# Optimization experiments

Hardware: AMD Instinct MI355X
Metric: run time of the kernel (lower is better)

The kernel has to match this reference:

```python
import jax, jax.numpy as jnp
import numpy as np

N, E, B, IN, H = 50000, 800000, 256, 1024, 256


def setup_inputs() -> dict:
    key = jax.random.key(0)
    ks = iter(jax.random.split(key, 40))
    w = lambda *s: jax.random.normal(next(ks), s, jnp.float32) * 0.05
    z = lambda *s: jnp.zeros(s, jnp.float32)
    inp = {
        "x": jax.random.normal(next(ks), (N, IN), jnp.float32),
        "edge_index": jax.random.randint(next(ks), (2, E), 0, N),
        "batch": jnp.sort(jax.random.randint(next(ks), (N,), 0, B)),
        "y": jax.random.randint(next(ks), (B,), 0, 2),
        "perm": jax.random.permutation(next(ks), B),
        # masker params
        "m_fc_w": w(IN, H), "m_fc_b": z(H),
        "m_c1_w": w(H, H), "m_c1_b": z(H),
        "m_c2_w": w(H, H), "m_c2_b": z(H),
        "m_node_w": w(H, 1), "m_node_b": z(1),
        "m_edge_w": w(2 * H, 1), "m_edge_b": z(1),
        # gnn_c params
        "c_fc_w": w(IN, H), "c_fc_b": z(H),
        "c_c1_w": w(H, H), "c_c1_b": z(H),
        "c_c2_w": w(H, H), "c_c2_b": z(H),
        # gnn_b params
        "b_fc_w": w(IN, H), "b_fc_b": z(H),
        "b_c1_w": w(H, H), "b_c1_b": z(H),
        "b_c2_w": w(H, H), "b_c2_b": z(H),
        # classifier heads
        "mlp_c_w": w(2 * H, 2), "mlp_c_b": z(2),
        "mlp_b_w": w(2 * H, 2), "mlp_b_b": z(2),
    }
    return inp


def _gcn_conv(x, w, b, row, col, ew):
    """PyG GCNConv: linear -> add self-loops -> sym-norm -> scatter-add -> bias."""
    n = x.shape[0]
    xw = x @ w
    loop = jnp.arange(n)
    r = jnp.concatenate([row, loop])
    c = jnp.concatenate([col, loop])
    if ew is None:
        ewf = jnp.ones(r.shape[0], xw.dtype)
    else:
        ewf = jnp.concatenate([ew, jnp.ones(n, xw.dtype)])
    deg = jax.ops.segment_sum(ewf, c, num_segments=n)
    dis = jnp.where(deg > 0, jax.lax.rsqrt(jnp.maximum(deg, 1e-12)), 0.0)
    norm = dis[r] * ewf * dis[c]
    out = jax.ops.segment_sum(xw[r] * norm[:, None], c, num_segments=n)
    return out + b


def _gnn_net(x, row, col, batch, node_mask, edge_mask, fc_w, fc_b, c1w, c1b, c2w, c2b):
    h = x * node_mask
    h = h @ fc_w + fc_b
    h = jax.nn.relu(_gcn_conv(h, c1w, c1b, row, col, edge_mask))
    h = jax.nn.relu(_gcn_conv(h, c2w, c2b, row, col, edge_mask))
    s = jax.ops.segment_sum(h, batch, num_segments=B)
    cnt = jax.ops.segment_sum(jnp.ones(h.shape[0], h.dtype), batch, num_segments=B)
    return s / jnp.maximum(cnt, 1.0)[:, None]


def _ce(logits, y):
    return -jnp.take_along_axis(jax.nn.log_softmax(logits, -1), y[:, None], 1)[:, 0]


def _gce(logits, y, q=0.7):
    p = jax.nn.softmax(logits, -1)
    yg = jnp.take_along_axis(p, y[:, None], 1)[:, 0]
    return _ce(logits, y) * (jax.lax.stop_gradient(yg) ** q) * q


def reference(x, edge_index, batch, y, perm,
              m_fc_w, m_fc_b, m_c1_w, m_c1_b, m_c2_w, m_c2_b,
              m_node_w, m_node_b, m_edge_w, m_edge_b,
              c_fc_w, c_fc_b, c_c1_w, c_c1_b, c_c2_w, c_c2_b,
              b_fc_w, b_fc_b, b_c1_w, b_c1_b, b_c2_w, b_c2_b,
              mlp_c_w, mlp_c_b, mlp_b_w, mlp_b_b):
    sg = jax.lax.stop_gradient
    row, col = edge_index[0], edge_index[1]

    # ---- GCNMasker (dropout = eval identity) ----
    h = x @ m_fc_w + m_fc_b
    h = jax.nn.relu(_gcn_conv(h, m_c1_w, m_c1_b, row, col, None))
    h = jax.nn.relu(_gcn_conv(h, m_c2_w, m_c2_b, row, col, None))
    node_score_c = jax.nn.sigmoid(h @ m_node_w + m_node_b)          # [N,1]
    # cat([x[row],x[col]]) @ W == (x @ W_top)[row] + (x @ W_bot)[col]
    es = (h @ m_edge_w[:H])[row] + (h @ m_edge_w[H:])[col] + m_edge_b
    edge_score_c = jax.nn.sigmoid(es)                               # [E,1]
    edge_score_b = 1.0 - edge_score_c
    node_score_b = 1.0 - node_score_c

    score_c = _gnn_net(x, row, col, batch, node_score_c, edge_score_c[:, 0],
                       c_fc_w, c_fc_b, c_c1_w, c_c1_b, c_c2_w, c_c2_b)  # [B,H]
    score_b = _gnn_net(x, row, col, batch, node_score_b, edge_score_b[:, 0],
                       b_fc_w, b_fc_b, b_c1_w, b_c1_b, b_c2_w, b_c2_b)  # [B,H]

    z_c = jnp.concatenate([score_c, sg(score_b)], axis=1)
    z_b = jnp.concatenate([sg(score_c), score_b], axis=1)
    pred_c = z_c @ mlp_c_w + mlp_c_b
    pred_b = z_b @ mlp_b_w + mlp_b_b

    loss_dis = _ce(pred_c, y).mean() + _gce(pred_b, y).mean()

    z_b_swap = score_b[perm]
    label_swap = y[perm]
    z_mix_conflict = jnp.concatenate([score_c, sg(z_b_swap)], axis=1)
    z_mix_align = jnp.concatenate([sg(score_c), z_b_swap], axis=1)
    pred_mix_conflict = z_mix_conflict @ mlp_c_w + mlp_c_b
    pred_mix_align = z_mix_align @ mlp_b_w + mlp_b_b
    loss_swap = _ce(pred_mix_conflict, y).mean() + _gce(pred_mix_align, label_swap).mean()

    lambda_swap = 15.0
    loss = loss_dis + lambda_swap * loss_swap
    return pred_c, loss
```

## Files before the change

kernel.cpp:

```cpp
#include <hip/hip_runtime.h>
#include <cstdint>
#include <cstddef>

#define N_NODES 50000
#define N_EDGES 800000
#define NB      256
#define IN_DIM  1024
#define HDIM    256

typedef __attribute__((ext_vector_type(8))) short bf16x8;
typedef __attribute__((ext_vector_type(4))) short s4v;
typedef __attribute__((ext_vector_type(4))) float f32x4;

__device__ __forceinline__ float sigmoidf_(float v) { return 1.0f / (1.0f + expf(-v)); }

__device__ __forceinline__ short f2bf(float f) {
    unsigned u = __float_as_uint(f);
    unsigned r = (u + 0x7FFFu + ((u >> 16) & 1u)) >> 16;
    return (short)r;
}
__device__ __forceinline__ float bf2f(short s) {
    return __uint_as_float(((unsigned)(unsigned short)s) << 16);
}

__global__ void k_hist(const int* __restrict__ col, int* __restrict__ cnt, int n) {
    int e = blockIdx.x * 256 + threadIdx.x;
    if (e < n) atomicAdd(&cnt[col[e]], 1);
}

__global__ void k_scan1(const int* __restrict__ cnt, int* __restrict__ ptr,
                        int* __restrict__ bsums, int n) {
    __shared__ int sh[256];
    int t = threadIdx.x;
    int base = blockIdx.x * 2048 + t * 8;
    int v[8]; int s = 0;
#pragma unroll
    for (int i = 0; i < 8; ++i) { int idx = base + i; v[i] = (idx < n) ? cnt[idx] : 0; s += v[i]; }
    sh[t] = s;
    __syncthreads();
    for (int off = 1; off < 256; off <<= 1) {
        int x = (t >= off) ? sh[t - off] : 0;
        __syncthreads();
        sh[t] += x;
        __syncthreads();
    }
    int excl = sh[t] - s;
    if (t == 255) bsums[blockIdx.x] = sh[255];
    int run = excl;
#pragma unroll
    for (int i = 0; i < 8; ++i) { int idx = base + i; if (idx < n) ptr[idx] = run; run += v[i]; }
}

__global__ void k_scan2(int* __restrict__ bsums, int nb, int* __restrict__ ptr_n) {
    if (threadIdx.x == 0 && blockIdx.x == 0) {
        int run = 0;
        for (int i = 0; i < nb; ++i) { int v = bsums[i]; bsums[i] = run; run += v; }
        ptr_n[0] = run;
    }
}

__global__ void k_scan3(int* __restrict__ ptr, const int* __restrict__ bsums, int n) {
    int base = blockIdx.x * 2048 + threadIdx.x * 8;
    int add = bsums[blockIdx.x];
#pragma unroll
    for (int i = 0; i < 8; ++i) { int idx = base + i; if (idx < n) ptr[idx] += add; }
}

__global__ void k_copy_int(const int* __restrict__ a, int* __restrict__ b, int n) {
    int i = blockIdx.x * 256 + threadIdx.x;
    if (i < n) b[i] = a[i];
}

__global__ void k_scatter(const int* __restrict__ row, const int* __restrict__ col,
                          int* __restrict__ fill, int* __restrict__ src,
                          int* __restrict__ eid, int n) {
    int e = blockIdx.x * 256 + threadIdx.x;
    if (e < n) {
        int c = col[e];
        int p = atomicAdd(&fill[c], 1);
        src[p] = row[e];
        eid[p] = e;
    }
}

__global__ void k_dis1(const int* __restrict__ ptr, float* __restrict__ dis, int n) {
    int i = blockIdx.x * 256 + threadIdx.x;
    if (i < n) {
        float deg = 1.0f + (float)(ptr[i + 1] - ptr[i]);
        dis[i] = 1.0f / sqrtf(deg);
    }
}

__global__ void k_splitB(const float* __restrict__ W, short* __restrict__ bt_hi,
                         short* __restrict__ bt_lo, int K, int nOff) {
    int idx = blockIdx.x * 256 + threadIdx.x;
    if (idx >= 256 * (K >> 2)) return;
    int n = idx & 255, kq = (idx >> 8) << 2;
    s4v h, l;
#pragma unroll
    for (int j = 0; j < 4; ++j) {
        float v = W[(size_t)(kq + j) * 256 + n];
        short hh = f2bf(v);
        h[j] = hh;
        l[j] = f2bf(v - bf2f(hh));
    }
    *reinterpret_cast<s4v*>(&bt_hi[(size_t)(nOff + n) * K + kq]) = h;
    *reinterpret_cast<s4v*>(&bt_lo[(size_t)(nOff + n) * K + kq]) = l;
}

template <int AMODE, int SCALE, int OUTK>
__global__ __launch_bounds__(256, 2) void k_gemm(const float* __restrict__ A32,
                                                 const short* __restrict__ AHg,
                                                 const short* __restrict__ ALg,
                                                 const short* __restrict__ BtHi,
                                                 const short* __restrict__ BtLo,
                                                 const float* __restrict__ nsv,
                                                 const float* __restrict__ kbias,
                                                 const float* __restrict__ cbias,
                                                 float* __restrict__ C32,
                                                 short* __restrict__ CHg,
                                                 short* __restrict__ CLg,
                                                 float* __restrict__ Cf1,
                                                 float* __restrict__ Cf2,
                                                 int M, int K) {
    __shared__ short Ah[128 * 32];
    __shared__ short Al[128 * 32];
    __shared__ short Bh[128 * 32];
    __shared__ short Bl[128 * 32];

    const int tid = threadIdx.x;
    const int lane = tid & 63;
    const int wave = tid >> 6;
    const int wr = wave >> 1, wc = wave & 1;
    const int lr = lane & 15, kg = lane >> 4;
    const int m0 = blockIdx.y * 128, n0 = blockIdx.x * 128;
    const int sw = (lr >> 1) & 3;

    f32x4 acc[4][4] = {};

    float4 pa[4]; float ps[4]; float4 pkb[4];
    int4 pah[2], pal[2];
    int4 pbh[2], pbl[2];

    const int NT = K >> 5;

    auto LOAD = [&](int t) {
        const int k0 = t << 5;
        if constexpr (AMODE == 0) {
#pragma unroll
            for (int i = 0; i < 4; ++i) {
                int u = tid + i * 256;
                int rowi = u >> 3, kq = (u & 7) << 2;
                int gr = m0 + rowi;
                float4 av = make_float4(0.f, 0.f, 0.f, 0.f);
                float s = 1.f;
                float4 kb = make_float4(0.f, 0.f, 0.f, 0.f);
                if (gr < M) {
                    av = *reinterpret_cast<const float4*>(A32 + (size_t)gr * K + k0 + kq);
                    if constexpr (SCALE == 1) s = nsv[gr];
                    if constexpr (SCALE == 2) s = 1.f - nsv[gr];
                    if constexpr (SCALE != 0)
                        kb = *reinterpret_cast<const float4*>(kbias + k0 + kq);
                }
                pa[i] = av; ps[i] = s; pkb[i] = kb;
            }
        } else {
#pragma unroll
            for (int i = 0; i < 2; ++i) {
                int u = tid + i * 256;
                int rowi = u >> 2, ch = u & 3;
                int gr = m0 + rowi;
                int4 h = make_int4(0, 0, 0, 0), l = make_int4(0, 0, 0, 0);
                if (gr < M) {
                    size_t g = (size_t)gr * K + k0 + (ch << 3);
                    h = *reinterpret_cast<const int4*>(AHg + g);
                    l = *reinterpret_cast<const int4*>(ALg + g);
                }
                pah[i] = h; pal[i] = l;
            }
        }
#pragma unroll
        for (int i = 0; i < 2; ++i) {
            int u = tid + i * 256;
            int rowi = u >> 2, ch = u & 3;
            size_t g = (size_t)(n0 + rowi) * K + k0 + (ch << 3);
            pbh[i] = *reinterpret_cast<const int4*>(BtHi + g);
            pbl[i] = *reinterpret_cast<const int4*>(BtLo + g);
        }
    };

    auto STORE = [&]() {
        if constexpr (AMODE == 0) {
#pragma unroll
            for (int i = 0; i < 4; ++i) {
                int u = tid + i * 256;
                int rowi = u >> 3, kq = (u & 7) << 2;
                float4 av = pa[i];
                if constexpr (SCALE != 0) {
                    float s = ps[i]; float4 kb = pkb[i];
                    av.x = fmaf(s, av.x, kb.x);
                    av.y = fmaf(s, av.y, kb.y);
                    av.z = fmaf(s, av.z, kb.z);
                    av.w = fmaf(s, av.w, kb.w);
                }
                short hx = f2bf(av.x), hy = f2bf(av.y), hz = f2bf(av.z), hw = f2bf(av.w);
                s4v h = {hx, hy, hz, hw};
                s4v l = {f2bf(av.x - bf2f(hx)), f2bf(av.y - bf2f(hy)),
                         f2bf(av.z - bf2f(hz)), f2bf(av.w - bf2f(hw))};
                int g = kq >> 3, hf = kq & 7;
                int base = rowi * 32 + ((g ^ ((rowi >> 1) & 3)) << 3) + hf;
                *reinterpret_cast<s4v*>(&Ah[base]) = h;
                *reinterpret_cast<s4v*>(&Al[base]) = l;
            }
        } else {
#pragma unroll
            for (int i = 0; i < 2; ++i) {
                int u = tid + i * 256;
                int rowi = u >> 2, ch = u & 3;
                int base = rowi * 32 + ((ch ^ ((rowi >> 1) & 3)) << 3);
                *reinterpret_cast<int4*>(&Ah[base]) = pah[i];
                *reinterpret_cast<int4*>(&Al[base]) = pal[i];
            }
        }
#pragma unroll
        for (int i = 0; i < 2; ++i) {
            int u = tid + i * 256;
            int rowi = u >> 2, ch = u & 3;
            int base = rowi * 32 + ((ch ^ ((rowi >> 1) & 3)) << 3);
            *reinterpret_cast<int4*>(&Bh[base]) = pbh[i];
            *reinterpret_cast<int4*>(&Bl[base]) = pbl[i];
        }
    };

    LOAD(0);
    STORE();
    __syncthreads();

    for (int t = 0; t < NT; ++t) {
        if (t + 1 < NT) LOAD(t + 1);

        bf16x8 a_h[4], a_l[4], b_h[4], b_l[4];
#pragma unroll
        for (int i = 0; i < 4; ++i) {
            int ar = wr * 64 + i * 16 + lr;
            int aoff = ar * 32 + ((kg ^ sw) << 3);
            a_h[i] = *reinterpret_cast<const bf16x8*>(&Ah[aoff]);
            a_l[i] = *reinterpret_cast<const bf16x8*>(&Al[aoff]);
            int br = wc * 64 + i * 16 + lr;
            int boff = br * 32 + ((kg ^ sw) << 3);
            b_h[i] = *reinterpret_cast<const bf16x8*>(&Bh[boff]);
            b_l[i] = *reinterpret_cast<const bf16x8*>(&Bl[boff]);
        }
#pragma unroll
        for (int i = 0; i < 4; ++i)
#pragma unroll
            for (int j = 0; j < 4; ++j) {
                acc[i][j] = __builtin_amdgcn_mfma_f32_16x16x32_bf16(a_h[i], b_h[j], acc[i][j], 0, 0, 0);
                acc[i][j] = __builtin_amdgcn_mfma_f32_16x16x32_bf16(a_h[i], b_l[j], acc[i][j], 0, 0, 0);
                acc[i][j] = __builtin_amdgcn_mfma_f32_16x16x32_bf16(a_l[i], b_h[j], acc[i][j], 0, 0, 0);
            }
        __syncthreads();
        if (t + 1 < NT) STORE();
        __syncthreads();
    }

#pragma unroll
    for (int i = 0; i < 4; ++i) {
#pragma unroll
        for (int j = 0; j < 4; ++j) {
#pragma unroll
            for (int r = 0; r < 4; ++r) {
                int gr = m0 + wr * 64 + i * 16 + kg * 4 + r;
                if (gr >= M) continue;
                int gc = n0 + wc * 64 + j * 16 + lr;
                float v = acc[i][j][r];
                if constexpr (OUTK == 0) {
                    C32[(size_t)gr * 256 + gc] = v;
                } else {
                    int seg = gc >> 8, c = gc & 255;
                    if (seg == 0) {
                        v += cbias[c];
                        short h = f2bf(v);
                        CHg[(size_t)gr * 256 + c] = h;
                        CLg[(size_t)gr * 256 + c] = f2bf(v - bf2f(h));
                    } else if (seg == 1) {
                        Cf1[(size_t)gr * 256 + c] = v;
                    } else {
                        Cf2[(size_t)gr * 256 + c] = v;
                    }
                }
            }
        }
    }
}

template <int MODE, int OUT>
__global__ __launch_bounds__(256) void k_conv(const float* __restrict__ xw,
                                              const float* __restrict__ dis,
                                              const float* __restrict__ ew,
                                              const int* __restrict__ ptr,
                                              const int* __restrict__ srcA,
                                              const int* __restrict__ eidA,
                                              const float* __restrict__ bias,
                                              float* __restrict__ out32,
                                              short* __restrict__ outH,
                                              short* __restrict__ outL) {
    int node = blockIdx.x * 4 + (threadIdx.x >> 6);
    if (node >= N_NODES) return;
    int lane = threadIdx.x & 63;
    const float4* xw4 = reinterpret_cast<const float4*>(xw);
    int s = ptr[node], e = ptr[node + 1];
    float4 acc = make_float4(0.f, 0.f, 0.f, 0.f);
    int k = s;
    for (; k + 2 <= e; k += 2) {
        int sr0 = srcA[k], sr1 = srcA[k + 1];
        float w0 = dis[sr0], w1 = dis[sr1];
        if (MODE == 1) { w0 *= ew[eidA[k]]; w1 *= ew[eidA[k + 1]]; }
        else if (MODE == 2) { w0 *= (1.0f - ew[eidA[k]]); w1 *= (1.0f - ew[eidA[k + 1]]); }
        float4 v0 = xw4[(size_t)sr0 * 64 + lane];
        float4 v1 = xw4[(size_t)sr1 * 64 + lane];
        acc.x = fmaf(w1, v1.x, fmaf(w0, v0.x, acc.x));
        acc.y = fmaf(w1, v1.y, fmaf(w0, v0.y, acc.y));
        acc.z = fmaf(w1, v1.z, fmaf(w0, v0.z, acc.z));
        acc.w = fmaf(w1, v1.w, fmaf(w0, v0.w, acc.w));
    }
    if (k < e) {
        int sr = srcA[k];
        float w = dis[sr];
        if (MODE == 1) w *= ew[eidA[k]];
        else if (MODE == 2) w *= (1.0f - ew[eidA[k]]);
        float4 v = xw4[(size_t)sr * 64 + lane];
        acc.x = fmaf(w, v.x, acc.x);
        acc.y = fmaf(w, v.y, acc.y);
        acc.z = fmaf(w, v.z, acc.z);
        acc.w = fmaf(w, v.w, acc.w);
    }
    float di = dis[node];
    float4 xv = xw4[(size_t)node * 64 + lane];
    float4 bv = reinterpret_cast<const float4*>(bias)[lane];
    float ox = fmaxf(fmaf(di, acc.x + di * xv.x, bv.x), 0.0f);
    float oy = fmaxf(fmaf(di, acc.y + di * xv.y, bv.y), 0.0f);
    float oz = fmaxf(fmaf(di, acc.z + di * xv.z, bv.z), 0.0f);
    float ow = fmaxf(fmaf(di, acc.w + di * xv.w, bv.w), 0.0f);
    size_t o4 = (size_t)node * 64 + lane;
    if constexpr (OUT == 0) {
        reinterpret_cast<float4*>(out32)[o4] = make_float4(ox, oy, oz, ow);
    } else {
        short hx = f2bf(ox), hy = f2bf(oy), hz = f2bf(oz), hw = f2bf(ow);
        s4v h = {hx, hy, hz, hw};
        s4v l = {f2bf(ox - bf2f(hx)), f2bf(oy - bf2f(hy)),
                 f2bf(oz - bf2f(hz)), f2bf(ow - bf2f(hw))};
        reinterpret_cast<s4v*>(outH)[o4] = h;
        reinterpret_cast<s4v*>(outL)[o4] = l;
    }
}

__global__ __launch_bounds__(256) void k_nodescore(const short* __restrict__ Sh,
                                                   const short* __restrict__ Sl,
                                                   const float* __restrict__ node_w,
                                                   const float* __restrict__ node_b,
                                                   const float* __restrict__ edge_w,
                                                   float* __restrict__ ns,
                                                   float* __restrict__ en1,
                                                   float* __restrict__ en2) {
    int node = blockIdx.x * 4 + (threadIdx.x >> 6);
    if (node >= N_NODES) return;
    int lane = threadIdx.x & 63;
    size_t o4 = (size_t)node * 64 + lane;
    s4v hh = reinterpret_cast<const s4v*>(Sh)[o4];
    s4v hl = reinterpret_cast<const s4v*>(Sl)[o4];
    float4 hv = make_float4(bf2f(hh[0]) + bf2f(hl[0]), bf2f(hh[1]) + bf2f(hl[1]),
                            bf2f(hh[2]) + bf2f(hl[2]), bf2f(hh[3]) + bf2f(hl[3]));
    float4 w1 = reinterpret_cast<const float4*>(node_w)[lane];
    float4 w2 = reinterpret_cast<const float4*>(edge_w)[lane];
    float4 w3 = reinterpret_cast<const float4*>(edge_w)[64 + lane];
    float d1 = hv.x * w1.x + hv.y * w1.y + hv.z * w1.z + hv.w * w1.w;
    float d2 = hv.x * w2.x + hv.y * w2.y + hv.z * w2.z + hv.w * w2.w;
    float d3 = hv.x * w3.x + hv.y * w3.y + hv.z * w3.z + hv.w * w3.w;
#pragma unroll
    for (int off = 32; off > 0; off >>= 1) {
        d1 += __shfl_xor(d1, off);
        d2 += __shfl_xor(d2, off);
        d3 += __shfl_xor(d3, off);
    }
    if (lane == 0) {
        ns[node] = sigmoidf_(d1 + node_b[0]);
        en1[node] = d2;
        en2[node] = d3;
    }
}

__global__ void k_edgescore(const int* __restrict__ row, const int* __restrict__ col,
                            const float* __restrict__ en1, const float* __restrict__ en2,
                            const float* __restrict__ eb, float* __restrict__ esc, int n) {
    int e = blockIdx.x * 256 + threadIdx.x;
    if (e < n) esc[e] = sigmoidf_(en1[row[e]] + en2[col[e]] + eb[0]);
}

__global__ void k_degcb(const int* __restrict__ ptr, const int* __restrict__ eidA,
                        const float* __restrict__ esc, float* __restrict__ dis_c,
                        float* __restrict__ dis_b, int n) {
    int i = blockIdx.x * 256 + threadIdx.x;
    if (i >= n) return;
    int s = ptr[i], e = ptr[i + 1];
    float t = 0.f;
    for (int k = s; k < e; ++k) t += esc[eidA[k]];
    float indeg = (float)(e - s);
    dis_c[i] = 1.0f / sqrtf(1.0f + t);
    dis_b[i] = 1.0f / sqrtf(1.0f + (indeg - t));
}

__global__ void k_starts(const int* __restrict__ batch, int* __restrict__ starts) {
    int b = threadIdx.x;
    if (b > NB) return;
    int lo = 0, hi = N_NODES;
    while (lo < hi) { int mid = (lo + hi) >> 1; if (batch[mid] < b) lo = mid + 1; else hi = mid; }
    starts[b] = lo;
}

__global__ __launch_bounds__(256) void k_pool(const float* __restrict__ h,
                                              const int* __restrict__ starts,
                                              float* __restrict__ out) {
    int b = blockIdx.x, ch = threadIdx.x;
    int s = starts[b], e = starts[b + 1];
    float acc = 0.f;
    for (int i = s; i < e; ++i) acc += h[(size_t)i * HDIM + ch];
    out[b * HDIM + ch] = acc / fmaxf((float)(e - s), 1.0f);
}

__global__ __launch_bounds__(64) void k_head(const float* __restrict__ score_c,
                                             const float* __restrict__ score_b,
                                             const int* __restrict__ y,
                                             const int* __restrict__ perm,
                                             const float* __restrict__ wc,
                                             const float* __restrict__ bc,
                                             const float* __restrict__ wb,
                                             const float* __restrict__ bb,
                                             float* __restrict__ pred_out,
                                             float* __restrict__ loss_part) {
    int b = blockIdx.x, lane = threadIdx.x;
    int pidx = perm[b];
    float4 vc = reinterpret_cast<const float4*>(score_c)[b * 64 + lane];
    float4 vb = reinterpret_cast<const float4*>(score_b)[b * 64 + lane];
    float4 vp = reinterpret_cast<const float4*>(score_b)[pidx * 64 + lane];
    const float4* wc4 = reinterpret_cast<const float4*>(wc);
    const float4* wb4 = reinterpret_cast<const float4*>(wb);
    float4 cA0 = wc4[lane * 2], cA1 = wc4[lane * 2 + 1];
    float4 cB0 = wc4[128 + lane * 2], cB1 = wc4[128 + lane * 2 + 1];
    float4 bA0 = wb4[lane * 2], bA1 = wb4[lane * 2 + 1];
    float4 bB0 = wb4[128 + lane * 2], bB1 = wb4[128 + lane * 2 + 1];

    float c1_0 = vc.x * cA0.x + vc.y * cA0.z + vc.z * cA1.x + vc.w * cA1.z;
    float c1_1 = vc.x * cA0.y + vc.y * cA0.w + vc.z * cA1.y + vc.w * cA1.w;
    float c2_0 = vb.x * cB0.x + vb.y * cB0.z + vb.z * cB1.x + vb.w * cB1.z;
    float c2_1 = vb.x * cB0.y + vb.y * cB0.w + vb.z * cB1.y + vb.w * cB1.w;
    float cp_0 = vp.x * cB0.x + vp.y * cB0.z + vp.z * cB1.x + vp.w * cB1.z;
    float cp_1 = vp.x * cB0.y + vp.y * cB0.w + vp.z * cB1.y + vp.w * cB1.w;
    float b1_0 = vc.x * bA0.x + vc.y * bA0.z + vc.z * bA1.x + vc.w * bA1.z;
    float b1_1 = vc.x * bA0.y + vc.y * bA0.w + vc.z * bA1.y + vc.w * bA1.w;
    float b2_0 = vb.x * bB0.x + vb.y * bB0.z + vb.z * bB1.x + vb.w * bB1.z;
    float b2_1 = vb.x * bB0.y + vb.y * bB0.w + vb.z * bB1.y + vb.w * bB1.w;
    float bp_0 = vp.x * bB0.x + vp.y * bB0.z + vp.z * bB1.x + vp.w * bB1.z;
    float bp_1 = vp.x * bB0.y + vp.y * bB0.w + vp.z * bB1.y + vp.w * bB1.w;

#pragma unroll
    for (int off = 32; off > 0; off >>= 1) {
        c1_0 += __shfl_xor(c1_0, off); c1_1 += __shfl_xor(c1_1, off);
        c2_0 += __shfl_xor(c2_0, off); c2_1 += __shfl_xor(c2_1, off);
        cp_0 += __shfl_xor(cp_0, off); cp_1 += __shfl_xor(cp_1, off);
        b1_0 += __shfl_xor(b1_0, off); b1_1 += __shfl_xor(b1_1, off);
        b2_0 += __shfl_xor(b2_0, off); b2_1 += __shfl_xor(b2_1, off);
        bp_0 += __shfl_xor(bp_0, off); bp_1 += __shfl_xor(bp_1, off);
    }
    if (lane == 0) {
        float pc0 = c1_0 + c2_0 + bc[0], pc1 = c1_1 + c2_1 + bc[1];
        float pb0 = b1_0 + b2_0 + bb[0], pb1 = b1_1 + b2_1 + bb[1];
        float pmc0 = c1_0 + cp_0 + bc[0], pmc1 = c1_1 + cp_1 + bc[1];
        float pma0 = b1_0 + bp_0 + bb[0], pma1 = b1_1 + bp_1 + bb[1];
        int yy = y[b], yp = y[pidx];

        float m1 = fmaxf(pc0, pc1);
        float lse1 = m1 + logf(expf(pc0 - m1) + expf(pc1 - m1));
        float ce_c = lse1 - (yy == 0 ? pc0 : pc1);
        float m2 = fmaxf(pb0, pb1);
        float lse2 = m2 + logf(expf(pb0 - m2) + expf(pb1 - m2));
        float ly2 = (yy == 0 ? pb0 : pb1);
        float gce_b = (lse2 - ly2) * powf(expf(ly2 - lse2), 0.7f) * 0.7f;
        float m3 = fmaxf(pmc0, pmc1);
        float lse3 = m3 + logf(expf(pmc0 - m3) + expf(pmc1 - m3));
        float ce_mc = lse3 - (yy == 0 ? pmc0 : pmc1);
        float m4 = fmaxf(pma0, pma1);
        float lse4 = m4 + logf(expf(pma0 - m4) + expf(pma1 - m4));
        float ly4 = (yp == 0 ? pma0 : pma1);
        float gce_ma = (lse4 - ly4) * powf(expf(ly4 - lse4), 0.7f) * 0.7f;

        loss_part[b] = (ce_c + gce_b + 15.0f * (ce_mc + gce_ma)) * (1.0f / (float)NB);
        pred_out[b * 2 + 0] = pc0;
        pred_out[b * 2 + 1] = pc1;
    }
}

__global__ void k_lossred(const float* __restrict__ part, float* __restrict__ out) {
    __shared__ float sh[256];
    int t = threadIdx.x;
    sh[t] = part[t];
    __syncthreads();
    for (int off = 128; off > 0; off >>= 1) {
        if (t < off) sh[t] += sh[t + off];
        __syncthreads();
    }
    if (t == 0) out[0] = sh[0];
}

extern "C" void kernel_launch(void* const* d_in, const int* in_sizes, int n_in,
                              void* d_out, int out_size, void* d_ws, size_t ws_size,
                              hipStream_t stream) {
    (void)in_sizes; (void)n_in; (void)out_size; (void)ws_size;
    const float* x      = (const float*)d_in[0];
    const int*   ei     = (const int*)d_in[1];
    const int*   batch  = (const int*)d_in[2];
    const int*   y      = (const int*)d_in[3];
    const int*   perm   = (const int*)d_in[4];
    const float* m_fc_w = (const float*)d_in[5],  *m_fc_b = (const float*)d_in[6];
    const float* m_c1_w = (const float*)d_in[7],  *m_c1_b = (const float*)d_in[8];
    const float* m_c2_w = (const float*)d_in[9],  *m_c2_b = (const float*)d_in[10];
    const float* m_nd_w = (const float*)d_in[11], *m_nd_b = (const float*)d_in[12];
    const float* m_ed_w = (const float*)d_in[13], *m_ed_b = (const float*)d_in[14];
    const float* c_fc_w = (const float*)d_in[15], *c_fc_b = (const float*)d_in[16];
    const float* c_c1_w = (const float*)d_in[17], *c_c1_b = (const float*)d_in[18];
    const float* c_c2_w = (const float*)d_in[19], *c_c2_b = (const float*)d_in[20];
    const float* b_fc_w = (const float*)d_in[21], *b_fc_b = (const float*)d_in[22];
    const float* b_c1_w = (const float*)d_in[23], *b_c1_b = (const float*)d_in[24];
    const float* b_c2_w = (const float*)d_in[25], *b_c2_b = (const float*)d_in[26];
    const float* mlp_c_w = (const float*)d_in[27], *mlp_c_b = (const float*)d_in[28];
    const float* mlp_b_w = (const float*)d_in[29], *mlp_b_b = (const float*)d_in[30];
    const int* row = ei;
    const int* col = ei + N_EDGES;

    char* p = (char*)d_ws;
    auto alloc = [&](size_t bytes) -> void* {
        uintptr_t q = ((uintptr_t)p + 255) & ~(uintptr_t)255;
        p = (char*)(q + bytes);
        return (void*)q;
    };
    short* S1h = (short*)alloc((size_t)N_NODES * HDIM * 2);
    short* S1l = (short*)alloc((size_t)N_NODES * HDIM * 2);
    float* Fc  = (float*)alloc((size_t)N_NODES * HDIM * 4);
    float* Fb  = (float*)alloc((size_t)N_NODES * HDIM * 4);
    float* Dv  = (float*)alloc((size_t)N_NODES * HDIM * 4);
    int* cnt    = (int*)alloc((size_t)N_NODES * 4);
    int* ptr    = (int*)alloc((size_t)(N_NODES + 1) * 4);
    int* bsums  = (int*)alloc(32 * 4);
    int* csrc   = (int*)alloc((size_t)N_EDGES * 4);
    int* ceid   = (int*)alloc((size_t)N_EDGES * 4);
    float* dis1 = (float*)alloc((size_t)N_NODES * 4);
    float* dis_c = (float*)alloc((size_t)N_NODES * 4);
    float* dis_b = (float*)alloc((size_t)N_NODES * 4);
    float* ns   = (float*)alloc((size_t)N_NODES * 4);
    float* en1  = (float*)alloc((size_t)N_NODES * 4);
    float* en2  = (float*)alloc((size_t)N_NODES * 4);
    float* esc  = (float*)alloc((size_t)N_EDGES * 4);
    float* sc   = (float*)alloc((size_t)NB * HDIM * 4);
    float* sb   = (float*)alloc((size_t)NB * HDIM * 4);
    int* starts = (int*)alloc((size_t)(NB + 1) * 4);
    float* lpart = (float*)alloc((size_t)NB * 4);
    short* wfch = (short*)alloc((size_t)768 * IN_DIM * 2);
    short* wfcl = (short*)alloc((size_t)768 * IN_DIM * 2);
    short* hw[6][2];
    for (int i = 0; i < 6; ++i) {
        hw[i][0] = (short*)alloc((size_t)256 * HDIM * 2);
        hw[i][1] = (short*)alloc((size_t)256 * HDIM * 2);
    }
    const float* hsrc[6] = {m_c1_w, m_c2_w, c_c1_w, c_c2_w, b_c1_w, b_c2_w};

    const int EB = N_EDGES / 256;
    const int NBk = (N_NODES + 255) / 256;
    const int NW = N_NODES / 4;
    const dim3 gFC(6, (N_NODES + 127) / 128);
    const dim3 gH(2, (N_NODES + 127) / 128);

    hipMemsetAsync(cnt, 0, (size_t)N_NODES * 4, stream);
    k_hist<<<EB, 256, 0, stream>>>(col, cnt, N_EDGES);
    k_scan1<<<25, 256, 0, stream>>>(cnt, ptr, bsums, N_NODES);
    k_scan2<<<1, 64, 0, stream>>>(bsums, 25, ptr + N_NODES);
    k_scan3<<<25, 256, 0, stream>>>(ptr, bsums, N_NODES);
    k_copy_int<<<NBk, 256, 0, stream>>>(ptr, cnt, N_NODES);
    k_scatter<<<EB, 256, 0, stream>>>(row, col, cnt, csrc, ceid, N_EDGES);
    k_dis1<<<NBk, 256, 0, stream>>>(ptr, dis1, N_NODES);
    k_starts<<<1, 512, 0, stream>>>(batch, starts);
    k_splitB<<<256, 256, 0, stream>>>(m_fc_w, wfch, wfcl, IN_DIM, 0);
    k_splitB<<<256, 256, 0, stream>>>(c_fc_w, wfch, wfcl, IN_DIM, 256);
    k_splitB<<<256, 256, 0, stream>>>(b_fc_w, wfch, wfcl, IN_DIM, 512);
    for (int i = 0; i < 6; ++i)
        k_splitB<<<64, 256, 0, stream>>>(hsrc[i], hw[i][0], hw[i][1], HDIM, 0);

    k_gemm<0, 0, 2><<<gFC, 256, 0, stream>>>(x, nullptr, nullptr, wfch, wfcl,
                                             nullptr, nullptr, m_fc_b,
                                             nullptr, S1h, S1l, Fc, Fb, N_NODES, IN_DIM);

    k_gemm<1, 0, 0><<<gH, 256, 0, stream>>>(nullptr, S1h, S1l, hw[0][0], hw[0][1],
                                            nullptr, nullptr, nullptr,
                                            Dv, nullptr, nullptr, nullptr, nullptr, N_NODES, HDIM);
    k_conv<0, 1><<<NW, 256, 0, stream>>>(Dv, dis1, nullptr, ptr, csrc, ceid, m_c1_b,
                                         nullptr, S1h, S1l);
    k_gemm<1, 0, 0><<<gH, 256, 0, stream>>>(nullptr, S1h, S1l, hw[1][0], hw[1][1],
                                            nullptr, nullptr, nullptr,
                                            Dv, nullptr, nullptr, nullptr, nullptr, N_NODES, HDIM);
    k_conv<0, 1><<<NW, 256, 0, stream>>>(Dv, dis1, nullptr, ptr, csrc, ceid, m_c2_b,
                                         nullptr, S1h, S1l);
    k_nodescore<<<NW, 256, 0, stream>>>(S1h, S1l, m_nd_w, m_nd_b, m_ed_w, ns, en1, en2);
    k_edgescore<<<EB, 256, 0, stream>>>(row, col, en1, en2, m_ed_b, esc, N_EDGES);
    k_degcb<<<NBk, 256, 0, stream>>>(ptr, ceid, esc, dis_c, dis_b, N_NODES);

    k_gemm<0, 1, 0><<<gH, 256, 0, stream>>>(Fc, nullptr, nullptr, hw[2][0], hw[2][1],
                                            ns, c_fc_b, nullptr,
                                            Dv, nullptr, nullptr, nullptr, nullptr, N_NODES, HDIM);
    k_conv<1, 1><<<NW, 256, 0, stream>>>(Dv, dis_c, esc, ptr, csrc, ceid, c_c1_b,
                                         nullptr, S1h, S1l);
    k_gemm<1, 0, 0><<<gH, 256, 0, stream>>>(nullptr, S1h, S1l, hw[3][0], hw[3][1],
                                            nullptr, nullptr, nullptr,
                                            Dv, nullptr, nullptr, nullptr, nullptr, N_NODES, HDIM);
    k_conv<1, 0><<<NW, 256, 0, stream>>>(Dv, dis_c, esc, ptr, csrc, ceid, c_c2_b,
                                         Fc, nullptr, nullptr);
    k_pool<<<NB, 256, 0, stream>>>(Fc, starts, sc);

    k_gemm<0, 2, 0><<<gH, 256, 0, stream>>>(Fb, nullptr, nullptr, hw[4][0], hw[4][1],
                                            ns, b_fc_b, nullptr,
                                            Dv, nullptr, nullptr, nullptr, nullptr, N_NODES, HDIM);
    k_conv<2, 1><<<NW, 256, 0, stream>>>(Dv, dis_b, esc, ptr, csrc, ceid, b_c1_b,
                                         nullptr, S1h, S1l);
    k_gemm<1, 0, 0><<<gH, 256, 0, stream>>>(nullptr, S1h, S1l, hw[5][0], hw[5][1],
                                            nullptr, nullptr, nullptr,
                                            Dv, nullptr, nullptr, nullptr, nullptr, N_NODES, HDIM);
    k_conv<2, 0><<<NW, 256, 0, stream>>>(Dv, dis_b, esc, ptr, csrc, ceid, b_c2_b,
                                         Fb, nullptr, nullptr);
    k_pool<<<NB, 256, 0, stream>>>(Fb, starts, sb);

    float* outp = (float*)d_out;
    k_head<<<NB, 64, 0, stream>>>(sc, sb, y, perm, mlp_c_w, mlp_c_b, mlp_b_w, mlp_b_b,
                                  outp, lpart);
    k_lossred<<<1, 256, 0, stream>>>(lpart, outp + NB * 2);
}
```

Measured before the change: 2.304 ms.

## Pre-split x to bf16 hi/lo, swizzle GEMM block order, unroll conv gather by 4

Three changes. First, a new pass splits x into bf16 hi/lo arrays once in workspace, so the first GEMM (six column blocks over x) reads pre-split data instead of re-converting fp32 tiles in every column block. Second, GEMM blocks are remapped to a grouped 1D order of 8-row groups to improve L2 reuse of A tiles. Third, the conv neighbour gather is unrolled by four to keep more loads in flight. The pre-split adds an extra write and read of x in bf16 and needs enough workspace, falling back to the old path otherwise.

```diff
diff --git a/kernel.cpp b/kernel.cpp
--- a/kernel.cpp
+++ b/kernel.cpp
@@ -106,6 +106,19 @@
     }
     *reinterpret_cast<s4v*>(&bt_hi[(size_t)(nOff + n) * K + kq]) = h;
     *reinterpret_cast<s4v*>(&bt_lo[(size_t)(nOff + n) * K + kq]) = l;
+}
+
+__global__ void k_splitX(const float* __restrict__ x, short* __restrict__ xh,
+                         short* __restrict__ xl) {
+    int idx = blockIdx.x * 256 + threadIdx.x;
+    if (idx >= N_NODES * (IN_DIM / 4)) return;
+    float4 v = reinterpret_cast<const float4*>(x)[idx];
+    short hx = f2bf(v.x), hy = f2bf(v.y), hz = f2bf(v.z), hw = f2bf(v.w);
+    s4v h = {hx, hy, hz, hw};
+    s4v l = {f2bf(v.x - bf2f(hx)), f2bf(v.y - bf2f(hy)),
+             f2bf(v.z - bf2f(hz)), f2bf(v.w - bf2f(hw))};
+    reinterpret_cast<s4v*>(xh)[idx] = h;
+    reinterpret_cast<s4v*>(xl)[idx] = l;
 }
 
 template <int AMODE, int SCALE, int OUTK>
@@ -122,7 +135,7 @@
                                                  short* __restrict__ CLg,
                                                  float* __restrict__ Cf1,
                                                  float* __restrict__ Cf2,
-                                                 int M, int K) {
+                                                 int M, int K, int NBX, int NBY) {
     __shared__ short Ah[128 * 32];
     __shared__ short Al[128 * 32];
     __shared__ short Bh[128 * 32];
@@ -133,7 +146,16 @@
     const int wave = tid >> 6;
     const int wr = wave >> 1, wc = wave & 1;
     const int lr = lane & 15, kg = lane >> 4;
-    const int m0 = blockIdx.y * 128, n0 = blockIdx.x * 128;
+
+    int bb = blockIdx.x;
+    int gpw = NBX << 3;
+    int g = bb / gpw;
+    int r = bb - g * gpw;
+    int rows_left = NBY - (g << 3);
+    int rem = rows_left < 8 ? rows_left : 8;
+    int by = (g << 3) + (r % rem);
+    int bx = r / rem;
+    const int m0 = by * 128, n0 = bx * 128;
     const int sw = (lr >> 1) & 3;
 
     f32x4 acc[4][4] = {};
@@ -172,9 +194,9 @@
                 int gr = m0 + rowi;
                 int4 h = make_int4(0, 0, 0, 0), l = make_int4(0, 0, 0, 0);
                 if (gr < M) {
-                    size_t g = (size_t)gr * K + k0 + (ch << 3);
-                    h = *reinterpret_cast<const int4*>(AHg + g);
-                    l = *reinterpret_cast<const int4*>(ALg + g);
+                    size_t gofs = (size_t)gr * K + k0 + (ch << 3);
+                    h = *reinterpret_cast<const int4*>(AHg + gofs);
+                    l = *reinterpret_cast<const int4*>(ALg + gofs);
                 }
                 pah[i] = h; pal[i] = l;
             }
@@ -183,9 +205,9 @@
         for (int i = 0; i < 2; ++i) {
             int u = tid + i * 256;
             int rowi = u >> 2, ch = u & 3;
-            size_t g = (size_t)(n0 + rowi) * K + k0 + (ch << 3);
-            pbh[i] = *reinterpret_cast<const int4*>(BtHi + g);
-            pbl[i] = *reinterpret_cast<const int4*>(BtLo + g);
+            size_t gofs = (size_t)(n0 + rowi) * K + k0 + (ch << 3);
+            pbh[i] = *reinterpret_cast<const int4*>(BtHi + gofs);
+            pbl[i] = *reinterpret_cast<const int4*>(BtLo + gofs);
         }
     };
 
@@ -207,8 +229,8 @@
                 s4v h = {hx, hy, hz, hw};
                 s4v l = {f2bf(av.x - bf2f(hx)), f2bf(av.y - bf2f(hy)),
                          f2bf(av.z - bf2f(hz)), f2bf(av.w - bf2f(hw))};
-                int g = kq >> 3, hf = kq & 7;
-                int base = rowi * 32 + ((g ^ ((rowi >> 1) & 3)) << 3) + hf;
+                int gq = kq >> 3, hf = kq & 7;
+                int base = rowi * 32 + ((gq ^ ((rowi >> 1) & 3)) << 3) + hf;
                 *reinterpret_cast<s4v*>(&Ah[base]) = h;
                 *reinterpret_cast<s4v*>(&Al[base]) = l;
             }
@@ -269,11 +291,11 @@
 #pragma unroll
         for (int j = 0; j < 4; ++j) {
 #pragma unroll
-            for (int r = 0; r < 4; ++r) {
-                int gr = m0 + wr * 64 + i * 16 + kg * 4 + r;
+            for (int r2 = 0; r2 < 4; ++r2) {
+                int gr = m0 + wr * 64 + i * 16 + kg * 4 + r2;
                 if (gr >= M) continue;
                 int gc = n0 + wc * 64 + j * 16 + lr;
-                float v = acc[i][j][r];
+                float v = acc[i][j][r2];
                 if constexpr (OUTK == 0) {
                     C32[(size_t)gr * 256 + gc] = v;
                 } else {
@@ -312,6 +334,25 @@
     int s = ptr[node], e = ptr[node + 1];
     float4 acc = make_float4(0.f, 0.f, 0.f, 0.f);
     int k = s;
+    for (; k + 4 <= e; k += 4) {
+        int sr0 = srcA[k], sr1 = srcA[k + 1], sr2 = srcA[k + 2], sr3 = srcA[k + 3];
+        float w0 = dis[sr0], w1 = dis[sr1], w2 = dis[sr2], w3 = dis[sr3];
+        if (MODE == 1) {
+            w0 *= ew[eidA[k]]; w1 *= ew[eidA[k + 1]];
+            w2 *= ew[eidA[k + 2]]; w3 *= ew[eidA[k + 3]];
+        } else if (MODE == 2) {
+            w0 *= (1.0f - ew[eidA[k]]); w1 *= (1.0f - ew[eidA[k + 1]]);
+            w2 *= (1.0f - ew[eidA[k + 2]]); w3 *= (1.0f - ew[eidA[k + 3]]);
+        }
+        float4 v0 = xw4[(size_t)sr0 * 64 + lane];
+        float4 v1 = xw4[(size_t)sr1 * 64 + lane];
+        float4 v2 = xw4[(size_t)sr2 * 64 + lane];
+        float4 v3 = xw4[(size_t)sr3 * 64 + lane];
+        acc.x = fmaf(w3, v3.x, fmaf(w2, v2.x, fmaf(w1, v1.x, fmaf(w0, v0.x, acc.x))));
+        acc.y = fmaf(w3, v3.y, fmaf(w2, v2.y, fmaf(w1, v1.y, fmaf(w0, v0.y, acc.y))));
+        acc.z = fmaf(w3, v3.z, fmaf(w2, v2.z, fmaf(w1, v1.z, fmaf(w0, v0.z, acc.z))));
+        acc.w = fmaf(w3, v3.w, fmaf(w2, v2.w, fmaf(w1, v1.w, fmaf(w0, v0.w, acc.w))));
+    }
     for (; k + 2 <= e; k += 2) {
         int sr0 = srcA[k], sr1 = srcA[k + 1];
         float w0 = dis[sr0], w1 = dis[sr1];
@@ -515,7 +556,7 @@
 extern "C" void kernel_launch(void* const* d_in, const int* in_sizes, int n_in,
                               void* d_out, int out_size, void* d_ws, size_t ws_size,
                               hipStream_t stream) {
-    (void)in_sizes; (void)n_in; (void)out_size; (void)ws_size;
+    (void)in_sizes; (void)n_in; (void)out_size;
     const float* x      = (const float*)d_in[0];
     const int*   ei     = (const int*)d_in[1];
     const int*   batch  = (const int*)d_in[2];
@@ -573,11 +614,21 @@
     }
     const float* hsrc[6] = {m_c1_w, m_c2_w, c_c1_w, c_c2_w, b_c1_w, b_c2_w};
 
+    size_t used = (size_t)(p - (char*)d_ws);
+    size_t xbytes = (size_t)N_NODES * IN_DIM * 2;
+    bool presplit = (used + 2 * xbytes + 1024) <= ws_size;
+    short* XHg = nullptr; short* XLg = nullptr;
+    if (presplit) {
+        XHg = (short*)alloc(xbytes);
+        XLg = (short*)alloc(xbytes);
+    }
+
     const int EB = N_EDGES / 256;
     const int NBk = (N_NODES + 255) / 256;
     const int NW = N_NODES / 4;
-    const dim3 gFC(6, (N_NODES + 127) / 128);
-    const dim3 gH(2, (N_NODES + 127) / 128);
+    const int NBY = (N_NODES + 127) / 128;
+    const int gFC = 6 * NBY;
+    const int gH  = 2 * NBY;
 
     hipMemsetAsync(cnt, 0, (size_t)N_NODES * 4, stream);
     k_hist<<<EB, 256, 0, stream>>>(col, cnt, N_EDGES);
@@ -594,18 +645,29 @@
     for (int i = 0; i < 6; ++i)
         k_splitB<<<64, 256, 0, stream>>>(hsrc[i], hw[i][0], hw[i][1], HDIM, 0);
 
-    k_gemm<0, 0, 2><<<gFC, 256, 0, stream>>>(x, nullptr, nullptr, wfch, wfcl,
-                                             nullptr, nullptr, m_fc_b,
-                                             nullptr, S1h, S1l, Fc, Fb, N_NODES, IN_DIM);
+    if (presplit) {
+        k_splitX<<<N_NODES, 256, 0, stream>>>(x, XHg, XLg);
+        k_gemm<1, 0, 2><<<gFC, 256, 0, stream>>>(nullptr, XHg, XLg, wfch, wfcl,
+                                                 nullptr, nullptr, m_fc_b,
+                                                 nullptr, S1h, S1l, Fc, Fb,
+                                                 N_NODES, IN_DIM, 6, NBY);
+    } else {
+        k_gemm<0, 0, 2><<<gFC, 256, 0, stream>>>(x, nullptr, nullptr, wfch, wfcl,
+                                                 nullptr, nullptr, m_fc_b,
+                                                 nullptr, S1h, S1l, Fc, Fb,
+                                                 N_NODES, IN_DIM, 6, NBY);
+    }
 
     k_gemm<1, 0, 0><<<gH, 256, 0, stream>>>(nullptr, S1h, S1l, hw[0][0], hw[0][1],
                                             nullptr, nullptr, nullptr,
-                                            Dv, nullptr, nullptr, nullptr, nullptr, N_NODES, HDIM);
+                                            Dv, nullptr, nullptr, nullptr, nullptr,
+                                            N_NODES, HDIM, 2, NBY);
     k_conv<0, 1><<<NW, 256, 0, stream>>>(Dv, dis1, nullptr, ptr, csrc, ceid, m_c1_b,
                                          nullptr, S1h, S1l);
     k_gemm<1, 0, 0><<<gH, 256, 0, stream>>>(nullptr, S1h, S1l, hw[1][0], hw[1][1],
                                             nullptr, nullptr, nullptr,
-                                            Dv, nullptr, nullptr, nullptr, nullptr, N_NODES, HDIM);
+                                            Dv, nullptr, nullptr, nullptr, nullptr,
+                                            N_NODES, HDIM, 2, NBY);
     k_conv<0, 1><<<NW, 256, 0, stream>>>(Dv, dis1, nullptr, ptr, csrc, ceid, m_c2_b,
                                          nullptr, S1h, S1l);
     k_nodescore<<<NW, 256, 0, stream>>>(S1h, S1l, m_nd_w, m_nd_b, m_ed_w, ns, en1, en2);
@@ -614,24 +676,28 @@
 
     k_gemm<0, 1, 0><<<gH, 256, 0, stream>>>(Fc, nullptr, nullptr, hw[2][0], hw[2][1],
                                             ns, c_fc_b, nullptr,
-                                            Dv, nullptr, nullptr, nullptr, nullptr, N_NODES, HDIM);
+                                            Dv, nullptr, nullptr, nullptr, nullptr,
+                                            N_NODES, HDIM, 2, NBY);
     k_conv<1, 1><<<NW, 256, 0, stream>>>(Dv, dis_c, esc, ptr, csrc, ceid, c_c1_b,
                                          nullptr, S1h, S1l);
     k_gemm<1, 0, 0><<<gH, 256, 0, stream>>>(nullptr, S1h, S1l, hw[3][0], hw[3][1],
                                             nullptr, nullptr, nullptr,
-                                            Dv, nullptr, nullptr, nullptr, nullptr, N_NODES, HDIM);
+                                            Dv, nullptr, nullptr, nullptr, nullptr,
+                                            N_NODES, HDIM, 2, NBY);
     k_conv<1, 0><<<NW, 256, 0, stream>>>(Dv, dis_c, esc, ptr, csrc, ceid, c_c2_b,
                                          Fc, nullptr, nullptr);
     k_pool<<<NB, 256, 0, stream>>>(Fc, starts, sc);
 
     k_gemm<0, 2, 0><<<gH, 256, 0, stream>>>(Fb, nullptr, nullptr, hw[4][0], hw[4][1],
                                             ns, b_fc_b, nullptr,
-                                            Dv, nullptr, nullptr, nullptr, nullptr, N_NODES, HDIM);
+                                            Dv, nullptr, nullptr, nullptr, nullptr,
+                                            N_NODES, HDIM, 2, NBY);
     k_conv<2, 1><<<NW, 256, 0, stream>>>(Dv, dis_b, esc, ptr, csrc, ceid, b_c1_b,
                                          nullptr, S1h, S1l);
     k_gemm<1, 0, 0><<<gH, 256, 0, stream>>>(nullptr, S1h, S1l, hw[5][0], hw[5][1],
                                             nullptr, nullptr, nullptr,
-                                            Dv, nullptr, nullptr, nullptr, nullptr, N_NODES, HDIM);
+                                            Dv, nullptr, nullptr, nullptr, nullptr,
+                                            N_NODES, HDIM, 2, NBY);
     k_conv<2, 0><<<NW, 256, 0, stream>>>(Dv, dis_b, esc, ptr, csrc, ceid, b_c2_b,
                                          Fb, nullptr, nullptr);
     k_pool<<<NB, 256, 0, stream>>>(Fb, starts, sb);
```

Result: no change. 2.337 ms (+1.4%).
